# Kernel tuning notes

Measured on AMD Instinct MI355X. Metric: run time of the kernel, lower is better.

Reference implementation:

```python
import math
import jax, jax.numpy as jnp
import numpy as np

Q = 24
N = 8
T_THETA = 1.0
R_S = 3.0
SIGMA_R = 1.0
RHO_MIN = 0.05
N_ORI = 4
TOL = 0.5


def _build_bank_7x7(n, tol=0.5, eps=1e-06):
    m = 3
    coords = np.arange(-m, m + 1, dtype=np.float32)
    u = coords.reshape(1, 1, 7)  # varies along width
    v = coords.reshape(1, 7, 1)  # varies along height
    Delta = math.pi / float(n)
    thetas = ((0.5 * Delta + np.arange(n, dtype=np.float32) * Delta) % math.pi).reshape(n, 1, 1)
    d = np.abs(-np.sin(thetas) * u + np.cos(thetas) * v)
    M = (d <= tol).astype(np.float32)
    M[:, m, m] = 1.0
    W = M[:, None, :, :]  # (n,1,7,7)
    denom = W.sum(axis=(1, 2, 3), keepdims=True) + eps
    return W / denom


def _bilinear_shift(Fm, dx, dy):
    """Shift-sample Fm (B,H,W) by (dx,dy) pixels, matching torch grid_sample
    (bilinear, zeros padding, align_corners=False) on linspace(-1,1) base grid."""
    B, H, W = Fm.shape
    xs = (jnp.arange(W, dtype=Fm.dtype) - dx) * (W / (W - 1)) - 0.5
    ys = (jnp.arange(H, dtype=Fm.dtype) - dy) * (H / (H - 1)) - 0.5

    def axis_parts(p, size):
        p0 = jnp.floor(p)
        f = p - p0
        i0 = p0.astype(jnp.int32)
        i1 = i0 + 1
        w0 = jnp.where((i0 >= 0) & (i0 < size), 1.0 - f, 0.0)
        w1 = jnp.where((i1 >= 0) & (i1 < size), f, 0.0)
        return jnp.clip(i0, 0, size - 1), jnp.clip(i1, 0, size - 1), w0, w1

    y0, y1, wy0, wy1 = axis_parts(ys, H)
    x0, x1, wx0, wx1 = axis_parts(xs, W)
    # separable bilinear: interpolate rows, then columns
    Fy = Fm[:, y0, :] * wy0[None, :, None] + Fm[:, y1, :] * wy1[None, :, None]
    return Fy[:, :, x0] * wx0[None, None, :] + Fy[:, :, x1] * wx1[None, None, :]


def _line_energy_theta(x):
    """x: (B,2,H,W) -> hat_theta (B,H,W) in [0, 2pi)."""
    Fm = jnp.sqrt(jnp.sum(x * x, axis=1))  # (B,H,W) L2 over channels
    t_n = jnp.arange(1, N + 1, dtype=x.dtype) / N * R_S
    w_n = jnp.exp(-t_n * t_n / (2.0 * SIGMA_R ** 2))
    w_n = w_n / w_n.sum()
    theta_q = 2.0 * jnp.pi * jnp.arange(Q, dtype=x.dtype) / Q
    cos_q, sin_q = jnp.cos(theta_q), jnp.sin(theta_q)

    def energy_one_angle(cs):
        c, s = cs
        # (N,B,H,W) samples along the ray, then radial weighted sum
        S = jax.vmap(lambda t: _bilinear_shift(Fm, t * c, t * s))(t_n)
        return jnp.tensordot(w_n, S, axes=1)  # (B,H,W)

    E = jax.lax.map(energy_one_angle, (cos_q, sin_q))  # (Q,B,H,W)
    pi_q = jax.nn.softmax(E / T_THETA, axis=0)
    sy = jnp.einsum('q,qbhw->bhw', sin_q, pi_q)
    cx = jnp.einsum('q,qbhw->bhw', cos_q, pi_q)
    hat = jnp.arctan2(sy, cx)
    return jnp.remainder(hat + 2.0 * jnp.pi, 2.0 * jnp.pi)


def setup_inputs() -> dict:
    key = jax.random.key(0)
    k1, = jax.random.split(key, 1)
    x = jax.random.normal(k1, (8, 2, 512, 512), dtype=jnp.float32)
    gain = jnp.ones((1,), dtype=jnp.float32)
    log_route_temp = jnp.asarray(math.log(0.08), dtype=jnp.float32)
    rho_scaled = (0.5 - RHO_MIN) / (1.0 - RHO_MIN)
    rho_logit = jnp.asarray(math.log(rho_scaled / (1.0 - rho_scaled)), dtype=jnp.float32)
    W_bank = jnp.asarray(_build_bank_7x7(N_ORI, tol=TOL))  # (4,1,7,7)
    Delta = math.pi / float(N_ORI)
    centers = (0.5 * Delta + np.arange(N_ORI, dtype=np.float32) * Delta).reshape(1, N_ORI, 1, 1)
    theta_centers = jnp.asarray(centers)
    return {"x": x, "gain": gain, "log_route_temp": log_route_temp,
            "rho_logit": rho_logit, "W_bank": W_bank, "theta_centers": theta_centers}


def reference(x, gain, log_route_temp, rho_logit, W_bank, theta_centers):
    hat_theta = _line_energy_theta(x)  # (B,H,W)
    # orientation bank conv: expand (n,1,7,7) -> (n,2,7,7), SAME padding (pad=3)
    w = jnp.broadcast_to(W_bank, (N_ORI, 2, 7, 7))
    y = jax.lax.conv_general_dilated(
        x, w, window_strides=(1, 1), padding=((3, 3), (3, 3)),
        dimension_numbers=('NCHW', 'OIHW', 'NCHW'))  # (B,n,H,W)
    # soft orientation routing
    theta = jnp.remainder(hat_theta, jnp.pi)[:, None, :, :]  # (B,1,H,W)
    delta = jnp.remainder(theta - theta_centers + 0.5 * jnp.pi, jnp.pi) - 0.5 * jnp.pi
    dist = jnp.abs(delta)  # (B,n,H,W)
    route_temp = jnp.clip(jnp.exp(log_route_temp), 0.001, 2.0)
    base = jax.nn.softmax(-dist / route_temp, axis=1)
    rho = jax.nn.sigmoid(rho_logit) * (1.0 - RHO_MIN) + RHO_MIN
    gamma = 1.0 / (rho + 1e-08)
    sharp = jnp.power(base + 1e-12, gamma)
    weights = sharp / (sharp.sum(axis=1, keepdims=True) + 1e-08)
    out = jnp.sum(y * weights, axis=1, keepdims=True)  # (B,1,H,W)
    return jnp.clip(gain, 0.001, None) * out
```

## Files before the change

### kernel.cpp

```cpp
#include <hip/hip_runtime.h>
#include <math.h>

#define HALO 4
#define TWX 72
#define TWY 12
#define NST (TWX*TWY)
#define QIW 528
#define QIH 520

typedef float f4 __attribute__((ext_vector_type(4)));

#if __has_builtin(__builtin_amdgcn_fractf)
#define FRACTF(x) __builtin_amdgcn_fractf(x)
#else
#define FRACTF(x) ((x) - floorf(x))
#endif
#if __has_builtin(__builtin_amdgcn_exp2f)
#define EXP2F(x) __builtin_amdgcn_exp2f(x)
#else
#define EXP2F(x) exp2f(x)
#endif
#if __has_builtin(__builtin_amdgcn_logf)
#define LOG2F(x) __builtin_amdgcn_logf(x)
#else
#define LOG2F(x) log2f(x)
#endif

__global__ __launch_bounds__(64) void gp_setup(const float* __restrict__ gain,
                                               const float* __restrict__ lrt,
                                               const float* __restrict__ rlg,
                                               const float* __restrict__ Wb,
                                               float* __restrict__ tbl) {
  int t = threadIdx.x;
  __shared__ float wtmp[8];
  if (t < 8) {
    float tn = (float)(t + 1) * 0.375f;
    wtmp[t] = expf(-0.5f * tn * tn);
  }
  if (t < 24) {
    float th = (6.283185307179586f * (float)t) / 24.0f;
    float c = cosf(th), s = sinf(th);
    const float sc = (float)(512.0 / 511.0);
    tbl[t] = c; tbl[24 + t] = s; tbl[48 + t] = c * sc; tbl[72 + t] = s * sc;
  }
  __syncthreads();
  if (t == 0) {
    const float L2E = 1.44269504088896340736f;
    float sum = 0.f;
    for (int n = 0; n < 8; ++n) sum += wtmp[n];
    for (int n = 0; n < 8; ++n) tbl[96 + n] = (wtmp[n] / sum) * L2E;
    float rt = expf(lrt[0]);
    rt = fminf(fmaxf(rt, 0.001f), 2.0f);
    float sg = 1.0f / (1.0f + expf(-rlg[0]));
    float rho = sg * 0.95f + 0.05f;
    tbl[104] = (1.0f / rt) * L2E;
    tbl[105] = 1.0f / (rho + 1e-8f);
    tbl[106] = fmaxf(gain[0], 0.001f);

    const int K0[7] = {14,15,23,24,25,33,34};
    const int K1[7] = {2,9,17,24,31,39,46};
    const int K2[7] = {4,11,17,24,31,37,44};
    const int K3[7] = {19,20,23,24,25,28,29};
    const int* KK[4] = {K0,K1,K2,K3};
    int ok = 1;
    for (int o = 0; o < 4; ++o) {
      float w0v = Wb[o * 49 + KK[o][0]];
      if (w0v == 0.f) ok = 0;
      unsigned long long mask = 0;
      for (int t2 = 0; t2 < 7; ++t2) mask |= 1ull << KK[o][t2];
      for (int k = 0; k < 49; ++k) {
        float w = Wb[o * 49 + k];
        int nz = (w != 0.f);
        int want = (int)((mask >> k) & 1ull);
        if (nz != want) ok = 0;
        if (nz && w != w0v) ok = 0;
      }
      tbl[180 + o] = w0v;
    }
    ((int*)tbl)[172] = ok;
  }
}

__device__ inline float fmv(const float* __restrict__ x0p, const float* __restrict__ x1p,
                            int Y, int X) {
  int cY = min(max(Y, 0), 511);
  int cX = min(max(X, 0), 511);
  size_t o = (size_t)cY * 512 + cX;
  float a = x0p[o], b = x1p[o];
  float f = sqrtf(a * a + b * b);
  return ((unsigned)X < 512u && (unsigned)Y < 512u) ? f : 0.f;
}

__global__ __launch_bounds__(256) void gp_quadF(const float* __restrict__ x,
                                                f4* __restrict__ qimg) {
  int g = blockIdx.x * 256 + threadIdx.x;
  if (g >= QIH * 132) return;
  int b = blockIdx.y;
  int y = g / 132, xg = g - y * 132;
  int X = xg * 4 - 4, Y = y - 4;
  const float* __restrict__ x0p = x + (size_t)b * 2 * 512 * 512;
  const float* __restrict__ x1p = x0p + 512 * 512;

  float F0[5], F1[5];
  if (X >= 0 && X <= 507 && Y >= 0 && Y <= 510) {
    size_t r0 = (size_t)Y * 512 + X, r1 = r0 + 512;
    f4 a0 = *(const f4*)(x0p + r0); float a4 = x0p[r0 + 4];
    f4 b0 = *(const f4*)(x1p + r0); float b4 = x1p[r0 + 4];
    f4 c0 = *(const f4*)(x0p + r1); float c4 = x0p[r1 + 4];
    f4 d0 = *(const f4*)(x1p + r1); float d4 = x1p[r1 + 4];
    #pragma unroll
    for (int i = 0; i < 4; ++i) {
      F0[i] = sqrtf(a0[i] * a0[i] + b0[i] * b0[i]);
      F1[i] = sqrtf(c0[i] * c0[i] + d0[i] * d0[i]);
    }
    F0[4] = sqrtf(a4 * a4 + b4 * b4);
    F1[4] = sqrtf(c4 * c4 + d4 * d4);
  } else {
    #pragma unroll
    for (int i = 0; i < 5; ++i) {
      F0[i] = fmv(x0p, x1p, Y, X + i);
      F1[i] = fmv(x0p, x1p, Y + 1, X + i);
    }
  }
  f4* dst = qimg + (size_t)(b * QIH + y) * QIW + xg * 4;
  #pragma unroll
  for (int k = 0; k < 4; ++k) {
    float d0 = F0[k + 1] - F0[k];
    f4 q;
    q[0] = F0[k];
    q[1] = d0;
    q[2] = F1[k] - F0[k];
    q[3] = (F1[k + 1] - F1[k]) - d0;
    dst[k] = q;
  }
}

__device__ inline float finish(float SY, float CX, float a0, float a1, float a2,
                               float a3, const float* __restrict__ cen,
                               float irt2, float gamma, float gainc) {
  const float TP  = 6.283185307179586f;
  const float PIF = 3.14159265358979323846f;
  const float HP  = 1.57079632679489661923f;
  float hat = atan2f(SY, CX);
  float r1 = hat + TP;
  r1 = (r1 >= TP) ? (r1 - TP) : r1;
  float theta = (r1 >= PIF) ? (r1 - PIF) : r1;
  float dist[4];
  #pragma unroll
  for (int o = 0; o < 4; ++o) {
    float d = theta - cen[o] + HP;
    d -= (d >= PIF) ? PIF : 0.f;
    d += (d < 0.f) ? PIF : 0.f;
    dist[o] = fabsf(d - HP);
  }
  float mn = fminf(fminf(dist[0], dist[1]), fminf(dist[2], dist[3]));
  float m2 = mn * irt2;
  float eo[4], Z = 0.f;
  #pragma unroll
  for (int o = 0; o < 4; ++o) { eo[o] = EXP2F(fmaf(-irt2, dist[o], m2)); Z += eo[o]; }
  float invZ = 1.0f / Z;
  float sh[4], Zs = 0.f;
  #pragma unroll
  for (int o = 0; o < 4; ++o) {
    sh[o] = EXP2F(gamma * LOG2F(fmaf(eo[o], invZ, 1e-12f)));
    Zs += sh[o];
  }
  float wsi = 1.0f / (Zs + 1e-8f);
  return gainc * ((a0 * sh[0] + a1 * sh[1] + a2 * sh[2] + a3 * sh[3]) * wsi);
}

#define TN0 0.375f
#define TN1 0.75f
#define TN2 1.125f
#define TN3 1.5f
#define TN4 1.875f
#define TN5 2.25f
#define TN6 2.625f
#define TN7 3.0f

#define CRD(n) \
  float px##n = fmaf(-cs, TN##n, axl); \
  float py##n = fmaf(-sn, TN##n, ayl); \
  int   ix##n = (int)px##n; \
  int   iy##n = (int)py##n; \
  float fx##n = FRACTF(px##n); \
  float fy##n = FRACTF(py##n);

#define BILERP(v, n) fmaf(fy##n, fmaf(fx##n, v.w, v.z), fmaf(fx##n, v.y, v.x))
#define BILERP4(v, n) fmaf(fy##n, fmaf(fx##n, v[3], v[2]), fmaf(fx##n, v[1], v[0]))

__global__ __launch_bounds__(256) void gp_main8(const float* __restrict__ x,
                                                const f4* __restrict__ qimg,
                                                const float* __restrict__ Wb,
                                                const float* __restrict__ cen,
                                                const float* __restrict__ tbl,
                                                float* __restrict__ out) {
  __shared__ f4    Qd[NST];
  __shared__ float Sm[NST];

  const int tx = threadIdx.x;
  const int ty = threadIdx.y;
  const int tid = ty * 64 + tx;
  int wg = blockIdx.x;
  int swz = (wg & 7) * 1024 + (wg >> 3);
  int bx = swz & 7;
  int by = (swz >> 3) & 127;
  int b  = swz >> 10;

  const int bx0 = bx * 64 - HALO;
  const int by0 = by * 4 - HALO;
  const float* __restrict__ x0p = x + (size_t)b * 2 * 512 * 512;
  const float* __restrict__ x1p = x0p + 512 * 512;
  const f4* __restrict__ qg = qimg + (size_t)(b * QIH + by * 4) * QIW + bx * 64;

  #pragma unroll
  for (int it = 0; it < 4; ++it) {
    int idx = tid + it * 256;
    if (idx < NST) {
      int r = idx / TWX, c = idx - r * TWX;
      Qd[idx] = qg[r * QIW + c];
    }
  }
  #pragma unroll
  for (int it = 0; it < 4; ++it) {
    int idx = tid + it * 256;
    if (idx < NST) {
      int r = idx / TWX, c = idx - r * TWX;
      int gy = by0 + r, gx = bx0 + c;
      float a = 0.f, bv = 0.f;
      if ((unsigned)gx < 512u && (unsigned)gy < 512u) {
        size_t o = (size_t)gy * 512 + gx;
        a = x0p[o]; bv = x1p[o];
      }
      Sm[idx] = a + bv;
    }
  }
  __syncthreads();

  const int gi = bx0 + HALO + tx;
  const int gj = by0 + HALO + ty;
  const float SC = (float)(512.0 / 511.0);
  const float axl = fmaf((float)gi, SC, -0.5f) - (float)bx0;
  const float ayl = fmaf((float)gj, SC, -0.5f) - (float)by0;

  const float wn0 = tbl[96], wn1 = tbl[97], wn2 = tbl[98], wn3 = tbl[99];
  const float wn4 = tbl[100], wn5 = tbl[101], wn6 = tbl[102], wn7 = tbl[103];

  float SY = 0.f, CX = 0.f;
  for (int q = 0; q < 24; ++q) {
    const float cs = tbl[48 + q];
    const float sn = tbl[72 + q];
    CRD(5) CRD(6) CRD(7)
    f4 B5 = qg[iy5 * QIW + ix5];
    f4 B6 = qg[iy6 * QIW + ix6];
    f4 B7 = qg[iy7 * QIW + ix7];
    CRD(0) CRD(1) CRD(2) CRD(3) CRD(4)
    f4 A0 = Qd[iy0 * TWX + ix0];
    f4 A1 = Qd[iy1 * TWX + ix1];
    f4 A2 = Qd[iy2 * TWX + ix2];
    f4 A3 = Qd[iy3 * TWX + ix3];
    f4 A4 = Qd[iy4 * TWX + ix4];
    float e2 = wn0 * BILERP4(A0, 0);
    e2 = fmaf(wn1, BILERP4(A1, 1), e2);
    e2 = fmaf(wn2, BILERP4(A2, 2), e2);
    e2 = fmaf(wn3, BILERP4(A3, 3), e2);
    e2 = fmaf(wn4, BILERP4(A4, 4), e2);
    asm volatile("" : : "v"(B5), "v"(B6), "v"(B7));
    e2 = fmaf(wn5, BILERP4(B5, 5), e2);
    e2 = fmaf(wn6, BILERP4(B6, 6), e2);
    e2 = fmaf(wn7, BILERP4(B7, 7), e2);

    float e = EXP2F(e2);
    SY = fmaf(e, tbl[24 + q], SY);
    CX = fmaf(e, tbl[q], CX);
  }

  const int* ti = (const int*)tbl;
  const int ccen = (ty + 4) * TWX + tx + 4;
  float a0, a1, a2, a3;
  if (ti[172]) {
    float sCt = Sm[ccen];
    float H3 = (Sm[ccen - 1] + sCt) + Sm[ccen + 1];
    float V3 = (Sm[ccen - TWX] + sCt) + Sm[ccen + TWX];
    a0 = tbl[180] * (H3 + ((Sm[ccen - 75] + Sm[ccen - 74]) + (Sm[ccen + 74] + Sm[ccen + 75])));
    a1 = tbl[181] * (V3 + ((Sm[ccen - 217] + Sm[ccen - 145]) + (Sm[ccen + 145] + Sm[ccen + 217])));
    a2 = tbl[182] * (V3 + ((Sm[ccen - 215] + Sm[ccen - 143]) + (Sm[ccen + 143] + Sm[ccen + 215])));
    a3 = tbl[183] * (H3 + ((Sm[ccen - 70] + Sm[ccen - 69]) + (Sm[ccen + 69] + Sm[ccen + 70])));
  } else {
    a0 = a1 = a2 = a3 = 0.f;
    for (int kj = 0; kj < 7; ++kj)
      for (int ki = 0; ki < 7; ++ki) {
        float s = Sm[(ty + 1 + kj) * TWX + (tx + 1 + ki)];
        int k = kj * 7 + ki;
        a0 = fmaf(s, Wb[k], a0); a1 = fmaf(s, Wb[49 + k], a1);
        a2 = fmaf(s, Wb[98 + k], a2); a3 = fmaf(s, Wb[147 + k], a3);
      }
  }

  const float irt2  = tbl[104];
  const float gamma = tbl[105];
  const float gainc = tbl[106];
  float ov = finish(SY, CX, a0, a1, a2, a3, cen, irt2, gamma, gainc);
  out[((size_t)b * 512 + gj) * 512 + gi] = ov;
}

__global__ __launch_bounds__(256) void gp_main_fb(const float* __restrict__ x,
                                                  const float* __restrict__ Wb,
                                                  const float* __restrict__ cen,
                                                  const float* __restrict__ tbl,
                                                  float* __restrict__ out) {
  __shared__ float Fm[NST];
  __shared__ float Sm[NST];
  __shared__ f4    Qd[NST];
  const int tx = threadIdx.x;
  const int ty = threadIdx.y;
  const int tid = ty * 64 + tx;
  const int bx0 = blockIdx.x * 64 - HALO;
  const int by0 = blockIdx.y * 4 - HALO;
  const int b = blockIdx.z;
  const float* __restrict__ x0p = x + (size_t)b * 2 * 512 * 512;
  const float* __restrict__ x1p = x0p + 512 * 512;
  #pragma unroll
  for (int it = 0; it < 4; ++it) {
    int idx = tid + it * 256;
    if (idx < NST) {
      int r = idx / TWX, c = idx - r * TWX;
      int gy = by0 + r, gx = bx0 + c;
      float a = 0.f, bv = 0.f;
      if ((unsigned)gx < 512u && (unsigned)gy < 512u) {
        size_t o = (size_t)gy * 512 + gx;
        a = x0p[o]; bv = x1p[o];
      }
      Fm[idx] = sqrtf(a * a + bv * bv);
      Sm[idx] = a + bv;
    }
  }
  __syncthreads();
  #pragma unroll
  for (int it = 0; it < 4; ++it) {
    int idx = tid + it * 256;
    if (idx < NST) {
      int r = idx / TWX, c = idx - r * TWX;
      int r1 = (r < TWY - 1) ? r + 1 : r;
      int c1 = (c < TWX - 1) ? c + 1 : c;
      float v00 = Fm[r * TWX + c],  v01 = Fm[r * TWX + c1];
      float v10 = Fm[r1 * TWX + c], v11 = Fm[r1 * TWX + c1];
      f4 qv; qv[0] = v00; qv[1] = v01 - v00; qv[2] = v10 - v00;
      qv[3] = (v11 - v10) - (v01 - v00);
      Qd[idx] = qv;
    }
  }
  __syncthreads();
  const int gi = bx0 + HALO + tx;
  const int gj = by0 + HALO + ty;
  const float SC = (float)(512.0 / 511.0);
  const float axl = fmaf((float)gi, SC, -0.5f) - (float)bx0;
  const float ayl = fmaf((float)gj, SC, -0.5f) - (float)by0;
  float wn[8];
  #pragma unroll
  for (int n = 0; n < 8; ++n) wn[n] = tbl[96 + n];
  float SY = 0.f, CX = 0.f;
  for (int q = 0; q < 24; ++q) {
    const float csx = tbl[48 + q];
    const float ssy = tbl[72 + q];
    float e2 = 0.f;
    #pragma unroll
    for (int n = 0; n < 8; ++n) {
      const float tn = 0.375f * (float)(n + 1);
      float px = fmaf(-csx, tn, axl);
      float py = fmaf(-ssy, tn, ayl);
      int ix = (int)px, iy = (int)py;
      float fx = FRACTF(px), fy = FRACTF(py);
      f4 v = Qd[iy * TWX + ix];
      float s = fmaf(fy, fmaf(fx, v[3], v[2]), fmaf(fx, v[1], v[0]));
      e2 = fmaf(wn[n], s, e2);
    }
    float e = EXP2F(e2);
    SY = fmaf(e, tbl[24 + q], SY);
    CX = fmaf(e, tbl[q], CX);
  }
  const int* ti = (const int*)tbl;
  const int ccen = (ty + 4) * TWX + tx + 4;
  float a0, a1, a2, a3;
  if (ti[172]) {
    float sCt = Sm[ccen];
    float H3 = (Sm[ccen - 1] + sCt) + Sm[ccen + 1];
    float V3 = (Sm[ccen - TWX] + sCt) + Sm[ccen + TWX];
    a0 = tbl[180] * (H3 + ((Sm[ccen - 75] + Sm[ccen - 74]) + (Sm[ccen + 74] + Sm[ccen + 75])));
    a1 = tbl[181] * (V3 + ((Sm[ccen - 217] + Sm[ccen - 145]) + (Sm[ccen + 145] + Sm[ccen + 217])));
    a2 = tbl[182] * (V3 + ((Sm[ccen - 215] + Sm[ccen - 143]) + (Sm[ccen + 143] + Sm[ccen + 215])));
    a3 = tbl[183] * (H3 + ((Sm[ccen - 70] + Sm[ccen - 69]) + (Sm[ccen + 69] + Sm[ccen + 70])));
  } else {
    a0 = a1 = a2 = a3 = 0.f;
    for (int kj = 0; kj < 7; ++kj)
      for (int ki = 0; ki < 7; ++ki) {
        float s = Sm[(ty + 1 + kj) * TWX + (tx + 1 + ki)];
        int k = kj * 7 + ki;
        a0 = fmaf(s, Wb[k], a0); a1 = fmaf(s, Wb[49 + k], a1);
        a2 = fmaf(s, Wb[98 + k], a2); a3 = fmaf(s, Wb[147 + k], a3);
      }
  }
  const float irt2  = tbl[104];
  const float gamma = tbl[105];
  const float gainc = tbl[106];
  float ov = finish(SY, CX, a0, a1, a2, a3, cen, irt2, gamma, gainc);
  out[((size_t)b * 512 + gj) * 512 + gi] = ov;
}

extern "C" void kernel_launch(void* const* d_in, const int* in_sizes, int n_in,
                              void* d_out, int out_size, void* d_ws, size_t ws_size,
                              hipStream_t stream) {
  const float* x    = (const float*)d_in[0];
  const float* gain = (const float*)d_in[1];
  const float* lrt  = (const float*)d_in[2];
  const float* rlg  = (const float*)d_in[3];
  const float* Wb   = (const float*)d_in[4];
  const float* cen  = (const float*)d_in[5];
  float* tbl = (float*)d_ws;

  gp_setup<<<1, 64, 0, stream>>>(gain, lrt, rlg, Wb, tbl);

  size_t need = 4096 + (size_t)8 * QIH * QIW * sizeof(f4);
  if (ws_size >= need) {
    f4* qimg = (f4*)((char*)d_ws + 4096);
    gp_quadF<<<dim3((QIH * 132 + 255) / 256, 8), 256, 0, stream>>>(x, qimg);
    gp_main8<<<dim3(8192), dim3(64, 4), 0, stream>>>(x, qimg, Wb, cen, tbl, (float*)d_out);
  } else {
    gp_main_fb<<<dim3(8, 128, 8), dim3(64, 4), 0, stream>>>(x, Wb, cen, tbl, (float*)d_out);
  }
}
```

Baseline: 151.7 us.

## Compute four rows per thread with taller 16-row tiles and shared x-coordinates

The main kernel now handles a 64x16 tile per block, with each thread computing four output rows spaced 4 apart. The x-sample coordinates and fractions are computed once per angle and reused across the four rows, and the shared-memory halo is amortised over four times as many outputs, so global staging traffic per pixel drops. The cost is higher register pressure from 12 in-flight global f4 loads and four accumulator pairs, hinted by launch_bounds(256,4), and a grid four times smaller, which may reduce occupancy and latency hiding.

Measured after the change: 160.4 us. +5.8%, slower.

```diff
diff --git a/kernel.cpp b/kernel.cpp
--- a/kernel.cpp
+++ b/kernel.cpp
@@ -3,8 +3,6 @@
 
 #define HALO 4
 #define TWX 72
-#define TWY 12
-#define NST (TWX*TWY)
 #define QIW 528
 #define QIH 520
 
@@ -178,53 +176,186 @@
 #define TN6 2.625f
 #define TN7 3.0f
 
-#define CRD(n) \
+#define XS(n) \
   float px##n = fmaf(-cs, TN##n, axl); \
-  float py##n = fmaf(-sn, TN##n, ayl); \
   int   ix##n = (int)px##n; \
-  int   iy##n = (int)py##n; \
-  float fx##n = FRACTF(px##n); \
-  float fy##n = FRACTF(py##n);
-
-#define BILERP(v, n) fmaf(fy##n, fmaf(fx##n, v.w, v.z), fmaf(fx##n, v.y, v.x))
-#define BILERP4(v, n) fmaf(fy##n, fmaf(fx##n, v[3], v[2]), fmaf(fx##n, v[1], v[0]))
-
-__global__ __launch_bounds__(256) void gp_main8(const float* __restrict__ x,
-                                                const f4* __restrict__ qimg,
-                                                const float* __restrict__ Wb,
-                                                const float* __restrict__ cen,
-                                                const float* __restrict__ tbl,
-                                                float* __restrict__ out) {
-  __shared__ f4    Qd[NST];
-  __shared__ float Sm[NST];
+  float fx##n = FRACTF(px##n);
+
+#define BISS(n,k) \
+  float pyB##n##k = fmaf(-sn, TN##n, ayl##k); \
+  int   iyB##n##k = (int)pyB##n##k; \
+  float fyB##n##k = FRACTF(pyB##n##k); \
+  f4    B##n##k   = qg[iyB##n##k * QIW + ix##n];
+
+#define ASMP(n,k) \
+  float pa##n##k = fmaf(-sn, TN##n, ayl##k); \
+  int   ia##n##k = (int)pa##n##k; \
+  float fa##n##k = FRACTF(pa##n##k); \
+  f4    A##n##k  = Qd[ia##n##k * 72 + ix##n];
+
+#define ABL(n,k) fmaf(fa##n##k, fmaf(fx##n, A##n##k[3], A##n##k[2]), fmaf(fx##n, A##n##k[1], A##n##k[0]))
+#define BBL(n,k) fmaf(fyB##n##k, fmaf(fx##n, B##n##k[3], B##n##k[2]), fmaf(fx##n, B##n##k[1], B##n##k[0]))
+
+#define AROW(k) \
+  ASMP(0,k) ASMP(1,k) ASMP(2,k) ASMP(3,k) ASMP(4,k) \
+  float e2##k = wn0 * ABL(0,k); \
+  e2##k = fmaf(wn1, ABL(1,k), e2##k); \
+  e2##k = fmaf(wn2, ABL(2,k), e2##k); \
+  e2##k = fmaf(wn3, ABL(3,k), e2##k); \
+  e2##k = fmaf(wn4, ABL(4,k), e2##k);
+
+#define BCONS(k) \
+  e2##k = fmaf(wn5, BBL(5,k), e2##k); \
+  e2##k = fmaf(wn6, BBL(6,k), e2##k); \
+  e2##k = fmaf(wn7, BBL(7,k), e2##k); \
+  { float e = EXP2F(e2##k); SY##k = fmaf(e, snq, SY##k); CX##k = fmaf(e, csq, CX##k); }
+
+__global__ __launch_bounds__(256, 4) void gp_main9(const f4* __restrict__ qimg,
+                                                   const float* __restrict__ x,
+                                                   const float* __restrict__ Wb,
+                                                   const float* __restrict__ cen,
+                                                   const float* __restrict__ tbl,
+                                                   float* __restrict__ out) {
+  __shared__ f4    Qd[24 * 72];
+  __shared__ float Sm[22 * 70];
 
   const int tx = threadIdx.x;
   const int ty = threadIdx.y;
   const int tid = ty * 64 + tx;
   int wg = blockIdx.x;
-  int swz = (wg & 7) * 1024 + (wg >> 3);
+  int swz = (wg & 7) * 256 + (wg >> 3);
   int bx = swz & 7;
-  int by = (swz >> 3) & 127;
-  int b  = swz >> 10;
-
-  const int bx0 = bx * 64 - HALO;
-  const int by0 = by * 4 - HALO;
+  int by = (swz >> 3) & 31;
+  int b  = swz >> 8;
+
   const float* __restrict__ x0p = x + (size_t)b * 2 * 512 * 512;
   const float* __restrict__ x1p = x0p + 512 * 512;
-  const f4* __restrict__ qg = qimg + (size_t)(b * QIH + by * 4) * QIW + bx * 64;
-
+  const f4* __restrict__ qg = qimg + (size_t)(b * QIH + by * 16) * QIW + bx * 64;
+
+  #pragma unroll
+  for (int it = 0; it < 7; ++it) {
+    int idx = tid + it * 256;
+    if (idx < 24 * 72) {
+      int r = idx / 72, c = idx - r * 72;
+      Qd[idx] = qg[r * QIW + c];
+    }
+  }
+  const int sy0 = by * 16 - 3, sx0 = bx * 64 - 3;
+  #pragma unroll
+  for (int it = 0; it < 7; ++it) {
+    int idx = tid + it * 256;
+    if (idx < 22 * 70) {
+      int r = idx / 70, c = idx - r * 70;
+      int gy = sy0 + r, gx = sx0 + c;
+      float a = 0.f, bv = 0.f;
+      if ((unsigned)gx < 512u && (unsigned)gy < 512u) {
+        size_t o = (size_t)gy * 512 + gx;
+        a = x0p[o]; bv = x1p[o];
+      }
+      Sm[idx] = a + bv;
+    }
+  }
+  __syncthreads();
+
+  const int gi = bx * 64 + tx;
+  const int gj0 = by * 16 + ty;
+  const float SC = (float)(512.0 / 511.0);
+  const float bx0f = (float)(bx * 64 - 4);
+  const float by0f = (float)(by * 16 - 4);
+  const float axl  = fmaf((float)gi, SC, -0.5f) - bx0f;
+  const float ayl0 = fmaf((float)gj0,        SC, -0.5f) - by0f;
+  const float ayl1 = fmaf((float)(gj0 + 4),  SC, -0.5f) - by0f;
+  const float ayl2 = fmaf((float)(gj0 + 8),  SC, -0.5f) - by0f;
+  const float ayl3 = fmaf((float)(gj0 + 12), SC, -0.5f) - by0f;
+
+  const float wn0 = tbl[96], wn1 = tbl[97], wn2 = tbl[98], wn3 = tbl[99];
+  const float wn4 = tbl[100], wn5 = tbl[101], wn6 = tbl[102], wn7 = tbl[103];
+
+  float SY0 = 0.f, CX0 = 0.f, SY1 = 0.f, CX1 = 0.f;
+  float SY2 = 0.f, CX2 = 0.f, SY3 = 0.f, CX3 = 0.f;
+
+  for (int q = 0; q < 24; ++q) {
+    const float cs = tbl[48 + q];
+    const float sn = tbl[72 + q];
+    const float csq = tbl[q];
+    const float snq = tbl[24 + q];
+    XS(0) XS(1) XS(2) XS(3) XS(4) XS(5) XS(6) XS(7)
+    BISS(5,0) BISS(5,1) BISS(5,2) BISS(5,3)
+    BISS(6,0) BISS(6,1) BISS(6,2) BISS(6,3)
+    BISS(7,0) BISS(7,1) BISS(7,2) BISS(7,3)
+    AROW(0) AROW(1) AROW(2) AROW(3)
+    asm volatile("" : : "v"(B50), "v"(B51), "v"(B52), "v"(B53),
+                        "v"(B60), "v"(B61), "v"(B62), "v"(B63),
+                        "v"(B70), "v"(B71), "v"(B72), "v"(B73));
+    BCONS(0) BCONS(1) BCONS(2) BCONS(3)
+  }
+
+  const int* ti = (const int*)tbl;
+  float a0k[4], a1k[4], a2k[4], a3k[4];
+  if (ti[172]) {
+    #pragma unroll
+    for (int k = 0; k < 4; ++k) {
+      int cc = (ty + 4 * k + 3) * 70 + tx + 3;
+      float sC = Sm[cc];
+      float H3 = (Sm[cc - 1] + sC) + Sm[cc + 1];
+      float V3 = (Sm[cc - 70] + sC) + Sm[cc + 70];
+      a0k[k] = tbl[180] * (H3 + ((Sm[cc - 73] + Sm[cc - 72]) + (Sm[cc + 72] + Sm[cc + 73])));
+      a1k[k] = tbl[181] * (V3 + ((Sm[cc - 211] + Sm[cc - 141]) + (Sm[cc + 141] + Sm[cc + 211])));
+      a2k[k] = tbl[182] * (V3 + ((Sm[cc - 209] + Sm[cc - 139]) + (Sm[cc + 139] + Sm[cc + 209])));
+      a3k[k] = tbl[183] * (H3 + ((Sm[cc - 68] + Sm[cc - 67]) + (Sm[cc + 67] + Sm[cc + 68])));
+    }
+  } else {
+    #pragma unroll
+    for (int k = 0; k < 4; ++k) { a0k[k] = a1k[k] = a2k[k] = a3k[k] = 0.f; }
+    for (int kj = 0; kj < 7; ++kj)
+      for (int ki = 0; ki < 7; ++ki) {
+        int kk = kj * 7 + ki;
+        float w0 = Wb[kk], w1 = Wb[49 + kk], w2 = Wb[98 + kk], w3 = Wb[147 + kk];
+        #pragma unroll
+        for (int k = 0; k < 4; ++k) {
+          float s = Sm[(ty + 4 * k + kj) * 70 + (tx + ki)];
+          a0k[k] = fmaf(s, w0, a0k[k]); a1k[k] = fmaf(s, w1, a1k[k]);
+          a2k[k] = fmaf(s, w2, a2k[k]); a3k[k] = fmaf(s, w3, a3k[k]);
+        }
+      }
+  }
+
+  const float irt2  = tbl[104];
+  const float gamma = tbl[105];
+  const float gainc = tbl[106];
+
+  float o0 = finish(SY0, CX0, a0k[0], a1k[0], a2k[0], a3k[0], cen, irt2, gamma, gainc);
+  float o1 = finish(SY1, CX1, a0k[1], a1k[1], a2k[1], a3k[1], cen, irt2, gamma, gainc);
+  float o2 = finish(SY2, CX2, a0k[2], a1k[2], a2k[2], a3k[2], cen, irt2, gamma, gainc);
+  float o3 = finish(SY3, CX3, a0k[3], a1k[3], a2k[3], a3k[3], cen, irt2, gamma, gainc);
+
+  size_t ob = ((size_t)b * 512 + gj0) * 512 + gi;
+  out[ob] = o0;
+  out[ob + 4 * 512] = o1;
+  out[ob + 8 * 512] = o2;
+  out[ob + 12 * 512] = o3;
+}
+
+__global__ __launch_bounds__(256) void gp_main_fb(const float* __restrict__ x,
+                                                  const float* __restrict__ Wb,
+                                                  const float* __restrict__ cen,
+                                                  const float* __restrict__ tbl,
+                                                  float* __restrict__ out) {
+  __shared__ float Fm[12 * TWX];
+  __shared__ float Sm[12 * TWX];
+  __shared__ f4    Qd[12 * TWX];
+  const int tx = threadIdx.x;
+  const int ty = threadIdx.y;
+  const int tid = ty * 64 + tx;
+  const int bx0 = blockIdx.x * 64 - HALO;
+  const int by0 = blockIdx.y * 4 - HALO;
+  const int b = blockIdx.z;
+  const float* __restrict__ x0p = x + (size_t)b * 2 * 512 * 512;
+  const float* __restrict__ x1p = x0p + 512 * 512;
   #pragma unroll
   for (int it = 0; it < 4; ++it) {
     int idx = tid + it * 256;
-    if (idx < NST) {
-      int r = idx / TWX, c = idx - r * TWX;
-      Qd[idx] = qg[r * QIW + c];
-    }
-  }
-  #pragma unroll
-  for (int it = 0; it < 4; ++it) {
-    int idx = tid + it * 256;
-    if (idx < NST) {
+    if (idx < 864) {
       int r = idx / TWX, c = idx - r * TWX;
       int gy = by0 + r, gx = bx0 + c;
       float a = 0.f, bv = 0.f;
@@ -232,49 +363,54 @@
         size_t o = (size_t)gy * 512 + gx;
         a = x0p[o]; bv = x1p[o];
       }
+      Fm[idx] = sqrtf(a * a + bv * bv);
       Sm[idx] = a + bv;
     }
   }
   __syncthreads();
-
+  #pragma unroll
+  for (int it = 0; it < 4; ++it) {
+    int idx = tid + it * 256;
+    if (idx < 864) {
+      int r = idx / TWX, c = idx - r * TWX;
+      int r1 = (r < 11) ? r + 1 : r;
+      int c1 = (c < TWX - 1) ? c + 1 : c;
+      float v00 = Fm[r * TWX + c],  v01 = Fm[r * TWX + c1];
+      float v10 = Fm[r1 * TWX + c], v11 = Fm[r1 * TWX + c1];
+      f4 qv; qv[0] = v00; qv[1] = v01 - v00; qv[2] = v10 - v00;
+      qv[3] = (v11 - v10) - (v01 - v00);
+      Qd[idx] = qv;
+    }
+  }
+  __syncthreads();
   const int gi = bx0 + HALO + tx;
   const int gj = by0 + HALO + ty;
   const float SC = (float)(512.0 / 511.0);
   const float axl = fmaf((float)gi, SC, -0.5f) - (float)bx0;
   const float ayl = fmaf((float)gj, SC, -0.5f) - (float)by0;
-
-  const float wn0 = tbl[96], wn1 = tbl[97], wn2 = tbl[98], wn3 = tbl[99];
-  const float wn4 = tbl[100], wn5 = tbl[101], wn6 = tbl[102], wn7 = tbl[103];
-
+  float wn[8];
+  #pragma unroll
+  for (int n = 0; n < 8; ++n) wn[n] = tbl[96 + n];
   float SY = 0.f, CX = 0.f;
   for (int q = 0; q < 24; ++q) {
-    const float cs = tbl[48 + q];
-    const float sn = tbl[72 + q];
-    CRD(5) CRD(6) CRD(7)
-    f4 B5 = qg[iy5 * QIW + ix5];
-    f4 B6 = qg[iy6 * QIW + ix6];
-    f4 B7 = qg[iy7 * QIW + ix7];
-    CRD(0) CRD(1) CRD(2) CRD(3) CRD(4)
-    f4 A0 = Qd[iy0 * TWX + ix0];
-    f4 A1 = Qd[iy1 * TWX + ix1];
-    f4 A2 = Qd[iy2 * TWX + ix2];
-    f4 A3 = Qd[iy3 * TWX + ix3];
-    f4 A4 = Qd[iy4 * TWX + ix4];
-    float e2 = wn0 * BILERP4(A0, 0);
-    e2 = fmaf(wn1, BILERP4(A1, 1), e2);
-    e2 = fmaf(wn2, BILERP4(A2, 2), e2);
-    e2 = fmaf(wn3, BILERP4(A3, 3), e2);
-    e2 = fmaf(wn4, BILERP4(A4, 4), e2);
-    asm volatile("" : : "v"(B5), "v"(B6), "v"(B7));
-    e2 = fmaf(wn5, BILERP4(B5, 5), e2);
-    e2 = fmaf(wn6, BILERP4(B6, 6), e2);
-    e2 = fmaf(wn7, BILERP4(B7, 7), e2);
-
+    const float csx = tbl[48 + q];
+    const float ssy = tbl[72 + q];
+    float e2 = 0.f;
+    #pragma unroll
+    for (int n = 0; n < 8; ++n) {
+      const float tn = 0.375f * (float)(n + 1);
+      float px = fmaf(-csx, tn, axl);
+      float py = fmaf(-ssy, tn, ayl);
+      int ix = (int)px, iy = (int)py;
+      float fx = FRACTF(px), fy = FRACTF(py);
+      f4 v = Qd[iy * TWX + ix];
+      float s = fmaf(fy, fmaf(fx, v[3], v[2]), fmaf(fx, v[1], v[0]));
+      e2 = fmaf(wn[n], s, e2);
+    }
     float e = EXP2F(e2);
     SY = fmaf(e, tbl[24 + q], SY);
     CX = fmaf(e, tbl[q], CX);
   }
-
   const int* ti = (const int*)tbl;
   const int ccen = (ty + 4) * TWX + tx + 4;
   float a0, a1, a2, a3;
@@ -296,110 +432,6 @@
         a2 = fmaf(s, Wb[98 + k], a2); a3 = fmaf(s, Wb[147 + k], a3);
       }
   }
-
-  const float irt2  = tbl[104];
-  const float gamma = tbl[105];
-  const float gainc = tbl[106];
-  float ov = finish(SY, CX, a0, a1, a2, a3, cen, irt2, gamma, gainc);
-  out[((size_t)b * 512 + gj) * 512 + gi] = ov;
-}
-
-__global__ __launch_bounds__(256) void gp_main_fb(const float* __restrict__ x,
-                                                  const float* __restrict__ Wb,
-                                                  const float* __restrict__ cen,
-                                                  const float* __restrict__ tbl,
-                                                  float* __restrict__ out) {
-  __shared__ float Fm[NST];
-  __shared__ float Sm[NST];
-  __shared__ f4    Qd[NST];
-  const int tx = threadIdx.x;
-  const int ty = threadIdx.y;
-  const int tid = ty * 64 + tx;
-  const int bx0 = blockIdx.x * 64 - HALO;
-  const int by0 = blockIdx.y * 4 - HALO;
-  const int b = blockIdx.z;
-  const float* __restrict__ x0p = x + (size_t)b * 2 * 512 * 512;
-  const float* __restrict__ x1p = x0p + 512 * 512;
-  #pragma unroll
-  for (int it = 0; it < 4; ++it) {
-    int idx = tid + it * 256;
-    if (idx < NST) {
-      int r = idx / TWX, c = idx - r * TWX;
-      int gy = by0 + r, gx = bx0 + c;
-      float a = 0.f, bv = 0.f;
-      if ((unsigned)gx < 512u && (unsigned)gy < 512u) {
-        size_t o = (size_t)gy * 512 + gx;
-        a = x0p[o]; bv = x1p[o];
-      }
-      Fm[idx] = sqrtf(a * a + bv * bv);
-      Sm[idx] = a + bv;
-    }
-  }
-  __syncthreads();
-  #pragma unroll
-  for (int it = 0; it < 4; ++it) {
-    int idx = tid + it * 256;
-    if (idx < NST) {
-      int r = idx / TWX, c = idx - r * TWX;
-      int r1 = (r < TWY - 1) ? r + 1 : r;
-      int c1 = (c < TWX - 1) ? c + 1 : c;
-      float v00 = Fm[r * TWX + c],  v01 = Fm[r * TWX + c1];
-      float v10 = Fm[r1 * TWX + c], v11 = Fm[r1 * TWX + c1];
-      f4 qv; qv[0] = v00; qv[1] = v01 - v00; qv[2] = v10 - v00;
-      qv[3] = (v11 - v10) - (v01 - v00);
-      Qd[idx] = qv;
-    }
-  }
-  __syncthreads();
-  const int gi = bx0 + HALO + tx;
-  const int gj = by0 + HALO + ty;
-  const float SC = (float)(512.0 / 511.0);
-  const float axl = fmaf((float)gi, SC, -0.5f) - (float)bx0;
-  const float ayl = fmaf((float)gj, SC, -0.5f) - (float)by0;
-  float wn[8];
-  #pragma unroll
-  for (int n = 0; n < 8; ++n) wn[n] = tbl[96 + n];
-  float SY = 0.f, CX = 0.f;
-  for (int q = 0; q < 24; ++q) {
-    const float csx = tbl[48 + q];
-    const float ssy = tbl[72 + q];
-    float e2 = 0.f;
-    #pragma unroll
-    for (int n = 0; n < 8; ++n) {
-      const float tn = 0.375f * (float)(n + 1);
-      float px = fmaf(-csx, tn, axl);
-      float py = fmaf(-ssy, tn, ayl);
-      int ix = (int)px, iy = (int)py;
-      float fx = FRACTF(px), fy = FRACTF(py);
-      f4 v = Qd[iy * TWX + ix];
-      float s = fmaf(fy, fmaf(fx, v[3], v[2]), fmaf(fx, v[1], v[0]));
-      e2 = fmaf(wn[n], s, e2);
-    }
-    float e = EXP2F(e2);
-    SY = fmaf(e, tbl[24 + q], SY);
-    CX = fmaf(e, tbl[q], CX);
-  }
-  const int* ti = (const int*)tbl;
-  const int ccen = (ty + 4) * TWX + tx + 4;
-  float a0, a1, a2, a3;
-  if (ti[172]) {
-    float sCt = Sm[ccen];
-    float H3 = (Sm[ccen - 1] + sCt) + Sm[ccen + 1];
-    float V3 = (Sm[ccen - TWX] + sCt) + Sm[ccen + TWX];
-    a0 = tbl[180] * (H3 + ((Sm[ccen - 75] + Sm[ccen - 74]) + (Sm[ccen + 74] + Sm[ccen + 75])));
-    a1 = tbl[181] * (V3 + ((Sm[ccen - 217] + Sm[ccen - 145]) + (Sm[ccen + 145] + Sm[ccen + 217])));
-    a2 = tbl[182] * (V3 + ((Sm[ccen - 215] + Sm[ccen - 143]) + (Sm[ccen + 143] + Sm[ccen + 215])));
-    a3 = tbl[183] * (H3 + ((Sm[ccen - 70] + Sm[ccen - 69]) + (Sm[ccen + 69] + Sm[ccen + 70])));
-  } else {
-    a0 = a1 = a2 = a3 = 0.f;
-    for (int kj = 0; kj < 7; ++kj)
-      for (int ki = 0; ki < 7; ++ki) {
-        float s = Sm[(ty + 1 + kj) * TWX + (tx + 1 + ki)];
-        int k = kj * 7 + ki;
-        a0 = fmaf(s, Wb[k], a0); a1 = fmaf(s, Wb[49 + k], a1);
-        a2 = fmaf(s, Wb[98 + k], a2); a3 = fmaf(s, Wb[147 + k], a3);
-      }
-  }
   const float irt2  = tbl[104];
   const float gamma = tbl[105];
   const float gainc = tbl[106];
@@ -424,7 +456,7 @@
   if (ws_size >= need) {
     f4* qimg = (f4*)((char*)d_ws + 4096);
     gp_quadF<<<dim3((QIH * 132 + 255) / 256, 8), 256, 0, stream>>>(x, qimg);
-    gp_main8<<<dim3(8192), dim3(64, 4), 0, stream>>>(x, qimg, Wb, cen, tbl, (float*)d_out);
+    gp_main9<<<dim3(2048), dim3(64, 4), 0, stream>>>(qimg, x, Wb, cen, tbl, (float*)d_out);
   } else {
     gp_main_fb<<<dim3(8, 128, 8), dim3(64, 4), 0, stream>>>(x, Wb, cen, tbl, (float*)d_out);
   }
```
